# Performance work log

Measured on AMD Instinct MI355X. Metric: run time of the kernel, lower is better.

Reference implementation:

```python
import jax, jax.numpy as jnp
import numpy as np

B, L, E, D = 4, 1024, 128, 256
NPOI, EPOI, NH, FF = 10000, 128, 8, 256
HD = D // NH


def layer_norm(x, g, b, eps=1e-5):
    m = x.mean(-1, keepdims=True)
    v = ((x - m) ** 2).mean(-1, keepdims=True)
    return (x - m) / jnp.sqrt(v + eps) * g + b


def leaky_relu(x):
    return jnp.where(x >= 0, x, 0.01 * x)


def tokenize_timestamp(t):
    # t: (..., 2) = [timestamp_sec, delta_sec] -> (..., 4) = [week, hour, minute, d_minute]
    week = t[..., 0] % 604800.0 / 86400.0
    hour = t[..., 0] % 86400.0 / 3600.0
    minute = t[..., 0] % 3600.0 / 60.0
    return jnp.stack([week, hour, minute, t[..., 1] / 60.0], -1)


def pos_encode(pos, d):
    # standard sinusoidal PE evaluated at integer positions `pos`
    freq = jnp.exp(-jnp.log(10000.0) * (2.0 * jnp.arange(d // 2, dtype=jnp.float32)) / d)
    ang = pos[..., None].astype(jnp.float32) * freq  # (..., d/2)
    pe = jnp.zeros(pos.shape + (d,), jnp.float32)
    return pe.at[..., 0::2].set(jnp.sin(ang)).at[..., 1::2].set(jnp.cos(ang))


def setup_inputs():
    ks = iter(jax.random.split(jax.random.key(0), 48))

    def nrm(shape, s=0.02):
        return jax.random.normal(next(ks), shape, jnp.float32) * s

    spatial = jax.random.normal(next(ks), (B, L, 2), jnp.float32) * 10.0
    ts = jax.random.uniform(next(ks), (B, L), jnp.float32, 0.0, 1e6)
    dt = jax.random.uniform(next(ks), (B, L), jnp.float32, 0.0, 3600.0)
    token = jax.random.randint(next(ks), (B, L, 2), 0, 2).astype(jnp.float32)
    iq = jnp.zeros((B, L, 4, 2), jnp.float32)
    iq = iq.at[..., 0, 0].set(spatial[..., 0]).at[..., 1, 0].set(spatial[..., 1])
    iq = iq.at[..., 2, 0].set(ts).at[..., 3, 0].set(dt)
    iq = iq.at[..., 0, 1].set(token[..., 0]).at[..., 2, 1].set(token[..., 1])
    positions = jax.random.randint(next(ks), (B, L, 2), 0, L)
    return dict(
        input_seq=iq, positions=positions,
        poi_coors=jax.random.normal(next(ks), (NPOI, 2), jnp.float32) * 10.0,
        poi_embed_mat=nrm((NPOI, EPOI), 1.0),
        sp_w1=nrm((2, E)), sp_b1=jnp.zeros((E,), jnp.float32),
        sp_w2=nrm((E, D)), sp_b2=jnp.zeros((D,), jnp.float32),
        four_w=nrm((4, E), 1.0), four_b=nrm((4, E), 1.0),
        te_w=nrm((4 * E, D)), te_b=jnp.zeros((D,), jnp.float32),
        poi_ln_g=jnp.ones((EPOI,), jnp.float32), poi_ln_b=jnp.zeros((EPOI,), jnp.float32),
        poi_w=nrm((EPOI, D)), poi_b=jnp.zeros((D,), jnp.float32),
        tok_emb=nrm((6, E), 1.0).at[5].set(0.0),
        tok_ln_g=jnp.ones((E,), jnp.float32), tok_ln_b=jnp.zeros((E,), jnp.float32),
        tok_w=nrm((E, D)), tok_b=jnp.zeros((D,), jnp.float32),
        mha_in_w=nrm((D, 3 * D)), mha_in_b=jnp.zeros((3 * D,), jnp.float32),
        mha_out_w=nrm((D, D)), mha_out_b=jnp.zeros((D,), jnp.float32),
        ln1_g=jnp.ones((D,), jnp.float32), ln1_b=jnp.zeros((D,), jnp.float32),
        ff_w1=nrm((D, FF)), ff_b1=jnp.zeros((FF,), jnp.float32),
        ff_w2=nrm((FF, D)), ff_b2=jnp.zeros((D,), jnp.float32),
        ln2_g=jnp.ones((D,), jnp.float32), ln2_b=jnp.zeros((D,), jnp.float32))


def reference(input_seq, positions, poi_coors, poi_embed_mat,
              sp_w1, sp_b1, sp_w2, sp_b2, four_w, four_b, te_w, te_b,
              poi_ln_g, poi_ln_b, poi_w, poi_b,
              tok_emb, tok_ln_g, tok_ln_b, tok_w, tok_b,
              mha_in_w, mha_in_b, mha_out_w, mha_out_b,
              ln1_g, ln1_b, ff_w1, ff_b1, ff_w2, ff_b2, ln2_g, ln2_b):
    token = input_seq[..., jnp.array([0, 2]), 1].astype(jnp.int32)  # (B,L,2)
    spatial = input_seq[:, :, 0:2, 0]                                # (B,L,2)
    tt = tokenize_timestamp(input_seq[:, :, 2:4, 0])                 # (B,L,4)
    # token embedding: Embedding(6) -> LN -> Linear -> (B,L,2,D)
    tok_e = layer_norm(tok_emb[token], tok_ln_g, tok_ln_b) @ tok_w + tok_b
    # spatial embedding (note: original's masked_fill is non-inplace and discarded)
    sp_e = leaky_relu(spatial @ sp_w1 + sp_b1) @ sp_w2 + sp_b2 + tok_e[:, :, 0]
    # brute-force nearest POI: cdist^2 + argmin + gather
    d2 = ((poi_coors[None, None] - spatial[:, :, None]) ** 2).sum(-1)  # (B,L,NPOI)
    poi = jnp.argmin(d2, -1)                                           # (B,L)
    poi_e = layer_norm(poi_embed_mat[poi], poi_ln_g, poi_ln_b) @ poi_w + poi_b + tok_e[:, :, 0]
    # temporal: 4 FourierEncode modules -> concat -> LeakyReLU -> Linear
    t_e = jnp.cos(tt[..., None] * four_w + four_b).reshape(B, L, 4 * E)
    t_e = leaky_relu(t_e) @ te_w + te_b + tok_e[:, :, 1]
    # modal mixer: 1-layer post-norm TransformerEncoder over the 3 modalities
    x = jnp.stack([sp_e, t_e, poi_e], 2).reshape(B * L, 3, D)
    qkv = x @ mha_in_w + mha_in_b
    q, k, v = jnp.split(qkv, 3, -1)
    q = q.reshape(B * L, 3, NH, HD)
    k = k.reshape(B * L, 3, NH, HD)
    v = v.reshape(B * L, 3, NH, HD)
    att = jax.nn.softmax(jnp.einsum('nqhd,nkhd->nhqk', q, k) / jnp.sqrt(jnp.float32(HD)), -1)
    o = jnp.einsum('nhqk,nkhd->nqhd', att, v).reshape(B * L, 3, D) @ mha_out_w + mha_out_b
    x = layer_norm(x + o, ln1_g, ln1_b)
    x = layer_norm(x + (jax.nn.relu(x @ ff_w1 + ff_b1) @ ff_w2 + ff_b2), ln2_g, ln2_b)
    modal_h = x.reshape(B, L, 3, D).mean(2)
    modal_h = modal_h + pos_encode(positions[..., 0], D) + pos_encode(positions[..., 1], D)
    return modal_h  # == mem_seq in the original forward
```

## Files before the change

### kernel.cpp

```cpp
#include <hip/hip_runtime.h>
#include <math.h>

namespace {
constexpr int E = 128, D = 256;
constexpr int NPOI = 10000, NH = 8, FFD = 256;
constexpr int HD = D / NH;
constexpr int NTOK = 4096;
constexpr int TA = 4;
constexpr float LN_EPS = 1e-5f;

constexpr int PK_QKV = 0;
constexpr int PK_OUT = 196608;
constexpr int PK_FF1 = 262144;
constexpr int PK_FF2 = 327680;
constexpr int PK_E0  = 393216;
constexpr int PK_E1  = 458752;
constexpr int PK_E2  = 622592;
constexpr int PK_TOTAL = 688128;
constexpr int NTILES = PK_TOTAL / 512;
}

using frag8 = __attribute__((ext_vector_type(8))) short;
using f32x4 = __attribute__((ext_vector_type(4))) float;

__device__ __forceinline__ float bf2f(short s) {
    union { unsigned u; float f; } x; x.u = ((unsigned)(unsigned short)s) << 16; return x.f;
}
__device__ __forceinline__ unsigned short f2bf(float f) {
    union { float f; unsigned u; } x; x.f = f;
    unsigned r = x.u + 0x7fffu + ((x.u >> 16) & 1u);
    return (unsigned short)(r >> 16);
}

__device__ __forceinline__ float wsum64(float v) {
#pragma unroll
    for (int m = 1; m < 64; m <<= 1) v += __shfl_xor(v, m);
    return v;
}

__device__ __forceinline__ void ln128_bf(const float* __restrict__ src,
                                         const float* __restrict__ g,
                                         const float* __restrict__ b,
                                         short* __restrict__ dst1,
                                         short* __restrict__ dst2, int lane) {
    float v0 = src[lane], v1 = src[64 + lane];
    float mean = wsum64(v0 + v1) * (1.0f / 128.0f);
    float d0 = v0 - mean, d1 = v1 - mean;
    float var = wsum64(d0 * d0 + d1 * d1) * (1.0f / 128.0f);
    float inv = sqrtf(var + LN_EPS);
    float y0 = d0 / inv * g[lane] + b[lane];
    float y1 = d1 / inv * g[64 + lane] + b[64 + lane];
    unsigned short s0 = f2bf(y0), s1 = f2bf(y1);
    dst1[lane] = (short)s0; dst1[64 + lane] = (short)s1;
    if (dst2) { dst2[lane] = (short)s0; dst2[64 + lane] = (short)s1; }
}

__global__ __launch_bounds__(256)
void pack_weights(const float* __restrict__ wqkv, const float* __restrict__ wout,
                  const float* __restrict__ fw1,  const float* __restrict__ fw2,
                  const float* __restrict__ sp_w2, const float* __restrict__ te_w,
                  const float* __restrict__ poi_w, const float* __restrict__ tok_w,
                  unsigned short* __restrict__ pk)
{
    __shared__ float buf[4][32 * 17];
    const int wv = threadIdx.x >> 6, lane = threadIdx.x & 63;
    const int tile = blockIdx.x * 4 + wv;
    if (tile >= NTILES) return;

    int t = tile, sel, base;
    if (t < 384)              { sel = 0; base = PK_QKV; }
    else if ((t -= 384) < 128){ sel = 1; base = PK_OUT; }
    else if ((t -= 128) < 128){ sel = 2; base = PK_FF1; }
    else if ((t -= 128) < 128){ sel = 3; base = PK_FF2; }
    else if ((t -= 128) < 128){ sel = 4; base = PK_E0; }
    else if ((t -= 128) < 320){ sel = 5; base = PK_E1; }
    else                      { t -= 320; sel = 6; base = PK_E2; }
    const int NKT = (sel == 5) ? 20 : 8;
    const int nt = t / NKT, kt = t % NKT;

    const int k = kt * 32 + (lane >> 1);
    const int n0 = nt * 16 + (lane & 1) * 8;
    const float* row;
    switch (sel) {
        case 0:  row = wqkv + (size_t)k * 768; break;
        case 1:  row = wout + (size_t)k * 256; break;
        case 2:  row = fw1  + (size_t)k * 256; break;
        case 3:  row = fw2  + (size_t)k * 256; break;
        case 4:  row = (k < 128) ? sp_w2 + (size_t)k * 256 : tok_w + (size_t)(k - 128) * 256; break;
        case 5:  row = (k < 512) ? te_w  + (size_t)k * 256 : tok_w + (size_t)(k - 512) * 256; break;
        default: row = (k < 128) ? poi_w + (size_t)k * 256 : tok_w + (size_t)(k - 128) * 256; break;
    }
    float4 v0 = *(const float4*)(row + n0);
    float4 v1 = *(const float4*)(row + n0 + 4);
    float* b = buf[wv];
    const int wb = (lane >> 1) * 17 + (lane & 1) * 8;
    b[wb + 0] = v0.x; b[wb + 1] = v0.y; b[wb + 2] = v0.z; b[wb + 3] = v0.w;
    b[wb + 4] = v1.x; b[wb + 5] = v1.y; b[wb + 6] = v1.z; b[wb + 7] = v1.w;
    __syncthreads();

    const int rb = (lane >> 4) * 8, c = lane & 15;
    frag8 fr;
#pragma unroll
    for (int j = 0; j < 8; ++j) fr[j] = (short)f2bf(b[(rb + j) * 17 + c]);
    *(frag8*)(pk + base + ((size_t)t * 64 + lane) * 8) = fr;
}

__global__ __launch_bounds__(256, 4)
void embed_mfma(const float* __restrict__ iq,
                const float* __restrict__ poi_coors,
                const float* __restrict__ poi_embed,
                const float* __restrict__ sp_w1, const float* __restrict__ sp_b1,
                const float* __restrict__ sp_b2,
                const float* __restrict__ four_w, const float* __restrict__ four_b,
                const float* __restrict__ te_b,
                const float* __restrict__ poi_ln_g, const float* __restrict__ poi_ln_b,
                const float* __restrict__ poi_b,
                const float* __restrict__ tok_emb,
                const float* __restrict__ tok_ln_g, const float* __restrict__ tok_ln_b,
                const float* __restrict__ tok_b,
                const unsigned short* __restrict__ pk,
                unsigned short* __restrict__ xout)
{
    constexpr int P0 = 264, P1 = 648, P2 = 264;
    const int tid = threadIdx.x;
    const int w = tid >> 6, lane = tid & 63;
    const int quad = lane >> 4, l16 = lane & 15;
    const int n0 = blockIdx.x * TA;

    __shared__ __align__(16) char  U[25088];
    __shared__ float s_meta[TA][6];
    __shared__ int   s_tok[TA][2];
    __shared__ float s_wd[4][TA];
    __shared__ int   s_wi[4][TA];
    __shared__ int   s_poi[TA];

    short* h0 = (short*)U;
    short* h1 = (short*)U + 1056;
    short* h2 = (short*)U + 3648;

    if (tid < TA) {
        const float* p = iq + (size_t)(n0 + tid) * 8;
        s_meta[tid][0] = p[0];
        s_meta[tid][1] = p[2];
        float ts = p[4];
        float dt = p[6];
        s_tok[tid][0] = (int)p[1];
        s_tok[tid][1] = (int)p[5];
        s_meta[tid][2] = fmodf(ts, 604800.0f) / 86400.0f;
        s_meta[tid][3] = fmodf(ts, 86400.0f) / 3600.0f;
        s_meta[tid][4] = fmodf(ts, 3600.0f) / 60.0f;
        s_meta[tid][5] = dt / 60.0f;
    }
    __syncthreads();

    {
        float sx[TA], sy[TA], bd[TA];
        int bi[TA];
#pragma unroll
        for (int t = 0; t < TA; ++t) {
            sx[t] = s_meta[t][0]; sy[t] = s_meta[t][1];
            bd[t] = INFINITY; bi[t] = NPOI;
        }
        const float2* pc = (const float2*)poi_coors;
        for (int i = tid; i < NPOI; i += 256) {
            float2 p = pc[i];
#pragma unroll
            for (int t = 0; t < TA; ++t) {
                float dx = __fsub_rn(p.x, sx[t]);
                float dy = __fsub_rn(p.y, sy[t]);
                float d  = __fadd_rn(__fmul_rn(dx, dx), __fmul_rn(dy, dy));
                if (d < bd[t]) { bd[t] = d; bi[t] = i; }
            }
        }
#pragma unroll
        for (int m = 1; m < 64; m <<= 1) {
#pragma unroll
            for (int t = 0; t < TA; ++t) {
                float od = __shfl_xor(bd[t], m);
                int   oi = __shfl_xor(bi[t], m);
                if (od < bd[t] || (od == bd[t] && oi < bi[t])) { bd[t] = od; bi[t] = oi; }
            }
        }
        if (lane == 0) {
#pragma unroll
            for (int t = 0; t < TA; ++t) { s_wd[w][t] = bd[t]; s_wi[w][t] = bi[t]; }
        }
        __syncthreads();
        if (tid < TA) {
            float bdd = s_wd[0][tid]; int bii = s_wi[0][tid];
#pragma unroll
            for (int ww = 1; ww < 4; ++ww) {
                float od = s_wd[ww][tid]; int oi = s_wi[ww][tid];
                if (od < bdd || (od == bdd && oi < bii)) { bdd = od; bii = oi; }
            }
            s_poi[tid] = bii;
        }
        __syncthreads();
    }

    {
        const int t = w;
        ln128_bf(tok_emb + (size_t)s_tok[t][0] * E, tok_ln_g, tok_ln_b,
                 h0 + t * P0 + 128, h2 + t * P2 + 128, lane);
        ln128_bf(tok_emb + (size_t)s_tok[t][1] * E, tok_ln_g, tok_ln_b,
                 h1 + t * P1 + 512, nullptr, lane);
        ln128_bf(poi_embed + (size_t)s_poi[t] * E, poi_ln_g, poi_ln_b,
                 h2 + t * P2, nullptr, lane);
    }

    for (int idx = tid; idx < TA * 128; idx += 256) {
        int t = idx >> 7, l = idx & 127;
        float h = s_meta[t][0] * sp_w1[l] + s_meta[t][1] * sp_w1[128 + l] + sp_b1[l];
        h0[t * P0 + l] = (short)f2bf((h >= 0.0f) ? h : 0.01f * h);
    }
    for (int idx = tid; idx < TA * 512; idx += 256) {
        int t = idx >> 9, jj = idx & 511, f = jj >> 7;
        float c = cosf(s_meta[t][2 + f] * four_w[jj] + four_b[jj]);
        h1[t * P1 + jj] = (short)f2bf((c >= 0.0f) ? c : 0.01f * c);
    }
    __syncthreads();

    {
        f32x4 acc[4];
#pragma unroll
        for (int nt = 0; nt < 4; ++nt) {
            int c = w * 64 + nt * 16 + l16;
            float bv = sp_b2[c] + tok_b[c];
            acc[nt][0] = bv; acc[nt][1] = bv; acc[nt][2] = bv; acc[nt][3] = bv;
        }
        for (int kt = 0; kt < 8; ++kt) {
            frag8 a = *(const frag8*)(&h0[l16 * P0 + kt * 32 + quad * 8]);
#pragma unroll
            for (int nt = 0; nt < 4; ++nt) {
                frag8 b = *(const frag8*)(pk + PK_E0 + (((size_t)(w * 4 + nt) * 8 + kt) * 64 + lane) * 8);
                acc[nt] = __builtin_amdgcn_mfma_f32_16x16x32_bf16(a, b, acc[nt], 0, 0, 0);
            }
        }
        if (quad == 0) {
#pragma unroll
            for (int nt = 0; nt < 4; ++nt)
#pragma unroll
                for (int r = 0; r < 4; ++r)
                    xout[(size_t)(n0 + r) * 768 + w * 64 + nt * 16 + l16] = f2bf(acc[nt][r]);
        }
    }
    {
        f32x4 acc[4];
#pragma unroll
        for (int nt = 0; nt < 4; ++nt) {
            int c = w * 64 + nt * 16 + l16;
            float bv = te_b[c] + tok_b[c];
            acc[nt][0] = bv; acc[nt][1] = bv; acc[nt][2] = bv; acc[nt][3] = bv;
        }
        for (int kt = 0; kt < 20; ++kt) {
            frag8 a = *(const frag8*)(&h1[l16 * P1 + kt * 32 + quad * 8]);
#pragma unroll
            for (int nt = 0; nt < 4; ++nt) {
                frag8 b = *(const frag8*)(pk + PK_E1 + (((size_t)(w * 4 + nt) * 20 + kt) * 64 + lane) * 8);
                acc[nt] = __builtin_amdgcn_mfma_f32_16x16x32_bf16(a, b, acc[nt], 0, 0, 0);
            }
        }
        if (quad == 0) {
#pragma unroll
            for (int nt = 0; nt < 4; ++nt)
#pragma unroll
                for (int r = 0; r < 4; ++r)
                    xout[(size_t)(n0 + r) * 768 + 256 + w * 64 + nt * 16 + l16] = f2bf(acc[nt][r]);
        }
    }
    {
        f32x4 acc[4];
#pragma unroll
        for (int nt = 0; nt < 4; ++nt) {
            int c = w * 64 + nt * 16 + l16;
            float bv = poi_b[c] + tok_b[c];
            acc[nt][0] = bv; acc[nt][1] = bv; acc[nt][2] = bv; acc[nt][3] = bv;
        }
        for (int kt = 0; kt < 8; ++kt) {
            frag8 a = *(const frag8*)(&h2[l16 * P2 + kt * 32 + quad * 8]);
#pragma unroll
            for (int nt = 0; nt < 4; ++nt) {
                frag8 b = *(const frag8*)(pk + PK_E2 + (((size_t)(w * 4 + nt) * 8 + kt) * 64 + lane) * 8);
                acc[nt] = __builtin_amdgcn_mfma_f32_16x16x32_bf16(a, b, acc[nt], 0, 0, 0);
            }
        }
        if (quad == 0) {
#pragma unroll
            for (int nt = 0; nt < 4; ++nt)
#pragma unroll
                for (int r = 0; r < 4; ++r)
                    xout[(size_t)(n0 + r) * 768 + 512 + w * 64 + nt * 16 + l16] = f2bf(acc[nt][r]);
        }
    }
}

__global__ __launch_bounds__(256, 3)
void mha_ff_mfma(const unsigned short* __restrict__ xin,
                 const unsigned short* __restrict__ pk,
                 const float* __restrict__ bqkv, const float* __restrict__ bout,
                 const float* __restrict__ ln1g, const float* __restrict__ ln1b,
                 const float* __restrict__ fb1,  const float* __restrict__ fb2,
                 const float* __restrict__ ln2g, const float* __restrict__ ln2b,
                 const int* __restrict__ positions,
                 float* __restrict__ out)
{
    constexpr int PA = 264;
    constexpr int PQ = 776;
    constexpr int PF = 260;
    const int tid = threadIdx.x;
    const int w = tid >> 6, lane = tid & 63;
    const int quad = lane >> 4, l16 = lane & 15;
    const int n0tok = blockIdx.x * TA;
    const unsigned short* xg = xin + (size_t)n0tok * 3 * D;

    __shared__ __align__(16) short s_a[16 * PA];
    __shared__ __align__(16) char  U[25088];
    __shared__ float s_att[TA * NH * 9];

    short* qkv = (short*)U;
    float* s_f = (float*)U;
    short* s_h = (short*)(U + 16640);

    for (int i = tid; i < 12 * 32; i += 256) {
        int row = i >> 5, col = (i & 31) * 8;
        *(frag8*)(&s_a[row * PA + col]) = *(const frag8*)(xg + row * 256 + col);
    }
    __syncthreads();

    float xres[16];

    {
        f32x4 acc[12];
#pragma unroll
        for (int nt = 0; nt < 12; ++nt) {
            float bv = bqkv[w * 192 + nt * 16 + l16];
            acc[nt][0] = bv; acc[nt][1] = bv; acc[nt][2] = bv; acc[nt][3] = bv;
        }
        for (int kt = 0; kt < 8; ++kt) {
            frag8 a = *(const frag8*)(&s_a[l16 * PA + kt * 32 + quad * 8]);
#pragma unroll
            for (int nt = 0; nt < 12; ++nt) {
                frag8 b = *(const frag8*)(pk + PK_QKV + (((size_t)(w * 12 + nt) * 8 + kt) * 64 + lane) * 8);
                acc[nt] = __builtin_amdgcn_mfma_f32_16x16x32_bf16(a, b, acc[nt], 0, 0, 0);
            }
        }
#pragma unroll
        for (int nt = 0; nt < 4; ++nt)
#pragma unroll
            for (int r = 0; r < 4; ++r)
                xres[nt * 4 + r] = bf2f(s_a[(quad * 4 + r) * PA + w * 64 + nt * 16 + l16]);
#pragma unroll
        for (int nt = 0; nt < 12; ++nt)
#pragma unroll
            for (int r = 0; r < 4; ++r) {
                int row = quad * 4 + r, col = w * 192 + nt * 16 + l16;
                qkv[row * PQ + col] = (short)f2bf(acc[nt][r]);
            }
    }
    __syncthreads();

    for (int idx = tid; idx < TA * NH * 9; idx += 256) {
        int tok = idx / 72, rem = idx % 72;
        int h = rem / 9, qr = (rem % 9) / 3, kr = rem % 3;
        const short* qp = qkv + (tok * 3 + qr) * PQ + h * HD;
        const short* kp = qkv + (tok * 3 + kr) * PQ + D + h * HD;
        float s = 0.0f;
#pragma unroll
        for (int u = 0; u < HD; ++u) s += bf2f(qp[u]) * bf2f(kp[u]);
        s_att[idx] = s / sqrtf((float)HD);
    }
    __syncthreads();
    for (int idx3 = tid; idx3 < TA * NH * 3; idx3 += 256) {
        float* a = s_att + idx3 * 3;
        float m = fmaxf(a[0], fmaxf(a[1], a[2]));
        float e0 = expf(a[0] - m), e1 = expf(a[1] - m), e2 = expf(a[2] - m);
        float inv = 1.0f / (e0 + e1 + e2);
        a[0] = e0 * inv; a[1] = e1 * inv; a[2] = e2 * inv;
    }
    __syncthreads();

    {
        const int h = tid >> 5;
#pragma unroll
        for (int tok = 0; tok < TA; ++tok) {
            float v0 = bf2f(qkv[(tok * 3 + 0) * PQ + 2 * D + tid]);
            float v1 = bf2f(qkv[(tok * 3 + 1) * PQ + 2 * D + tid]);
            float v2 = bf2f(qkv[(tok * 3 + 2) * PQ + 2 * D + tid]);
#pragma unroll
            for (int qr = 0; qr < 3; ++qr) {
                const float* a = s_att + tok * 72 + h * 9 + qr * 3;
                s_a[(tok * 3 + qr) * PA + tid] = (short)f2bf(a[0] * v0 + a[1] * v1 + a[2] * v2);
            }
        }
    }
    __syncthreads();

    {
        f32x4 acc[4];
#pragma unroll
        for (int nt = 0; nt < 4; ++nt) {
            float bv = bout[w * 64 + nt * 16 + l16];
            acc[nt][0] = bv; acc[nt][1] = bv; acc[nt][2] = bv; acc[nt][3] = bv;
        }
        for (int kt = 0; kt < 8; ++kt) {
            frag8 a = *(const frag8*)(&s_a[l16 * PA + kt * 32 + quad * 8]);
#pragma unroll
            for (int nt = 0; nt < 4; ++nt) {
                frag8 b = *(const frag8*)(pk + PK_OUT + (((size_t)(w * 4 + nt) * 8 + kt) * 64 + lane) * 8);
                acc[nt] = __builtin_amdgcn_mfma_f32_16x16x32_bf16(a, b, acc[nt], 0, 0, 0);
            }
        }
        __syncthreads();
#pragma unroll
        for (int nt = 0; nt < 4; ++nt)
#pragma unroll
            for (int r = 0; r < 4; ++r) {
                int row = quad * 4 + r, col = w * 64 + nt * 16 + l16;
                s_f[row * PF + col] = acc[nt][r] + xres[nt * 4 + r];
            }
    }
    __syncthreads();

#pragma unroll
    for (int rr = 0; rr < 4; ++rr) {
        int row = w + rr * 4, col = lane * 4;
        float4 v = *(const float4*)(&s_f[row * PF + col]);
        float mean = wsum64(v.x + v.y + v.z + v.w) * (1.0f / 256.0f);
        float dx = v.x - mean, dy = v.y - mean, dz = v.z - mean, dw = v.w - mean;
        float var = wsum64(dx * dx + dy * dy + dz * dz + dw * dw) * (1.0f / 256.0f);
        float s = sqrtf(var + LN_EPS);
        float4 g = *(const float4*)(ln1g + col), b = *(const float4*)(ln1b + col);
        float y0 = dx / s * g.x + b.x, y1 = dy / s * g.y + b.y;
        float y2 = dz / s * g.z + b.z, y3 = dw / s * g.w + b.w;
        float4 yv; yv.x = y0; yv.y = y1; yv.z = y2; yv.w = y3;
        *(float4*)(&s_f[row * PF + col]) = yv;
        ushort4 bb; bb.x = f2bf(y0); bb.y = f2bf(y1); bb.z = f2bf(y2); bb.w = f2bf(y3);
        *(ushort4*)(&s_a[row * PA + col]) = bb;
    }
    __syncthreads();

    {
        f32x4 acc[4];
#pragma unroll
        for (int nt = 0; nt < 4; ++nt) {
            float bv = fb1[w * 64 + nt * 16 + l16];
            acc[nt][0] = bv; acc[nt][1] = bv; acc[nt][2] = bv; acc[nt][3] = bv;
        }
        for (int kt = 0; kt < 8; ++kt) {
            frag8 a = *(const frag8*)(&s_a[l16 * PA + kt * 32 + quad * 8]);
#pragma unroll
            for (int nt = 0; nt < 4; ++nt) {
                frag8 b = *(const frag8*)(pk + PK_FF1 + (((size_t)(w * 4 + nt) * 8 + kt) * 64 + lane) * 8);
                acc[nt] = __builtin_amdgcn_mfma_f32_16x16x32_bf16(a, b, acc[nt], 0, 0, 0);
            }
        }
#pragma unroll
        for (int nt = 0; nt < 4; ++nt)
#pragma unroll
            for (int r = 0; r < 4; ++r) {
                int row = quad * 4 + r, col = w * 64 + nt * 16 + l16;
                s_h[row * PA + col] = (short)f2bf(fmaxf(acc[nt][r], 0.0f));
            }
    }
    __syncthreads();

    {
        f32x4 acc[4];
#pragma unroll
        for (int nt = 0; nt < 4; ++nt) {
            float bv = fb2[w * 64 + nt * 16 + l16];
            acc[nt][0] = bv; acc[nt][1] = bv; acc[nt][2] = bv; acc[nt][3] = bv;
        }
        for (int kt = 0; kt < 8; ++kt) {
            frag8 a = *(const frag8*)(&s_h[l16 * PA + kt * 32 + quad * 8]);
#pragma unroll
            for (int nt = 0; nt < 4; ++nt) {
                frag8 b = *(const frag8*)(pk + PK_FF2 + (((size_t)(w * 4 + nt) * 8 + kt) * 64 + lane) * 8);
                acc[nt] = __builtin_amdgcn_mfma_f32_16x16x32_bf16(a, b, acc[nt], 0, 0, 0);
            }
        }
#pragma unroll
        for (int nt = 0; nt < 4; ++nt)
#pragma unroll
            for (int r = 0; r < 4; ++r) {
                int row = quad * 4 + r, col = w * 64 + nt * 16 + l16;
                float y = s_f[row * PF + col];
                s_f[row * PF + col] = acc[nt][r] + y;
            }
    }
    __syncthreads();

#pragma unroll
    for (int rr = 0; rr < 4; ++rr) {
        int row = w + rr * 4, col = lane * 4;
        float4 v = *(const float4*)(&s_f[row * PF + col]);
        float mean = wsum64(v.x + v.y + v.z + v.w) * (1.0f / 256.0f);
        float dx = v.x - mean, dy = v.y - mean, dz = v.z - mean, dw = v.w - mean;
        float var = wsum64(dx * dx + dy * dy + dz * dz + dw * dw) * (1.0f / 256.0f);
        float s = sqrtf(var + LN_EPS);
        float4 g = *(const float4*)(ln2g + col), b = *(const float4*)(ln2b + col);
        float4 zv;
        zv.x = dx / s * g.x + b.x; zv.y = dy / s * g.y + b.y;
        zv.z = dz / s * g.z + b.z; zv.w = dw / s * g.w + b.w;
        *(float4*)(&s_f[row * PF + col]) = zv;
    }
    __syncthreads();

    {
        const int fi = tid >> 1;
        const float freq = expf(-logf(10000.0f) * (2.0f * fi) / (float)D);
#pragma unroll
        for (int t = 0; t < TA; ++t) {
            int n = n0tok + t;
            float m3 = (s_f[(3 * t) * PF + tid] + s_f[(3 * t + 1) * PF + tid] +
                        s_f[(3 * t + 2) * PF + tid]) / 3.0f;
            float p0 = (float)positions[2 * n], p1 = (float)positions[2 * n + 1];
            float a0 = p0 * freq, a1 = p1 * freq;
            float pe = (tid & 1) ? (cosf(a0) + cosf(a1)) : (sinf(a0) + sinf(a1));
            out[(size_t)n * D + tid] = m3 + pe;
        }
    }
}

extern "C" void kernel_launch(void* const* d_in, const int* in_sizes, int n_in,
                              void* d_out, int out_size, void* d_ws, size_t ws_size,
                              hipStream_t stream)
{
    const float* iq        = (const float*)d_in[0];
    const int*   positions = (const int*)d_in[1];
    const float* poi_coors = (const float*)d_in[2];
    const float* poi_embed = (const float*)d_in[3];
    const float* sp_w1     = (const float*)d_in[4];
    const float* sp_b1     = (const float*)d_in[5];
    const float* sp_w2     = (const float*)d_in[6];
    const float* sp_b2     = (const float*)d_in[7];
    const float* four_w    = (const float*)d_in[8];
    const float* four_b    = (const float*)d_in[9];
    const float* te_w      = (const float*)d_in[10];
    const float* te_b      = (const float*)d_in[11];
    const float* poi_ln_g  = (const float*)d_in[12];
    const float* poi_ln_b  = (const float*)d_in[13];
    const float* poi_w     = (const float*)d_in[14];
    const float* poi_b     = (const float*)d_in[15];
    const float* tok_emb   = (const float*)d_in[16];
    const float* tok_ln_g  = (const float*)d_in[17];
    const float* tok_ln_b  = (const float*)d_in[18];
    const float* tok_w     = (const float*)d_in[19];
    const float* tok_b     = (const float*)d_in[20];
    const float* mha_in_w  = (const float*)d_in[21];
    const float* mha_in_b  = (const float*)d_in[22];
    const float* mha_out_w = (const float*)d_in[23];
    const float* mha_out_b = (const float*)d_in[24];
    const float* ln1_g     = (const float*)d_in[25];
    const float* ln1_b     = (const float*)d_in[26];
    const float* ff_w1     = (const float*)d_in[27];
    const float* ff_b1     = (const float*)d_in[28];
    const float* ff_w2     = (const float*)d_in[29];
    const float* ff_b2     = (const float*)d_in[30];
    const float* ln2_g     = (const float*)d_in[31];
    const float* ln2_b     = (const float*)d_in[32];

    unsigned short* pkw = (unsigned short*)d_ws;
    unsigned short* xws = (unsigned short*)((char*)d_ws + PK_TOTAL * 2);

    pack_weights<<<NTILES / 4, 256, 0, stream>>>(
        mha_in_w, mha_out_w, ff_w1, ff_w2, sp_w2, te_w, poi_w, tok_w, pkw);

    embed_mfma<<<NTOK / TA, 256, 0, stream>>>(
        iq, poi_coors, poi_embed, sp_w1, sp_b1, sp_b2, four_w, four_b, te_b,
        poi_ln_g, poi_ln_b, poi_b, tok_emb, tok_ln_g, tok_ln_b, tok_b,
        pkw, xws);

    mha_ff_mfma<<<NTOK / TA, 256, 0, stream>>>(
        xws, pkw, mha_in_b, mha_out_b, ln1_g, ln1_b,
        ff_b1, ff_b2, ln2_g, ln2_b, positions, (float*)d_out);
}
```

Measured before the change: 213.2 us.

## Stage embed output in LDS, fuse score+softmax, raise mha occupancy bound

The embedding kernel now writes its bf16 outputs into a shared-memory tile and then stores them to global memory with coalesced 16-byte vector writes, replacing scattered 2-byte stores. The attention score loop now has each thread compute all three key scores for a query and apply the softmax immediately, which removes one barrier and a shared-memory round trip. The MHA/FF kernel's launch bounds go from 3 to 4 waves per SIMD, which may push the compiler to spill registers. The extra LDS buffer adds about 6 KB per block in the embed kernel.

```diff
diff --git a/kernel.cpp b/kernel.cpp
--- a/kernel.cpp
+++ b/kernel.cpp
@@ -128,6 +128,7 @@
     const int n0 = blockIdx.x * TA;
 
     __shared__ __align__(16) char  U[25088];
+    __shared__ __align__(16) short s_x[TA * 768];
     __shared__ float s_meta[TA][6];
     __shared__ int   s_tok[TA][2];
     __shared__ float s_wd[4][TA];
@@ -241,7 +242,7 @@
             for (int nt = 0; nt < 4; ++nt)
 #pragma unroll
                 for (int r = 0; r < 4; ++r)
-                    xout[(size_t)(n0 + r) * 768 + w * 64 + nt * 16 + l16] = f2bf(acc[nt][r]);
+                    s_x[r * 768 + w * 64 + nt * 16 + l16] = (short)f2bf(acc[nt][r]);
         }
     }
     {
@@ -265,7 +266,7 @@
             for (int nt = 0; nt < 4; ++nt)
 #pragma unroll
                 for (int r = 0; r < 4; ++r)
-                    xout[(size_t)(n0 + r) * 768 + 256 + w * 64 + nt * 16 + l16] = f2bf(acc[nt][r]);
+                    s_x[r * 768 + 256 + w * 64 + nt * 16 + l16] = (short)f2bf(acc[nt][r]);
         }
     }
     {
@@ -289,12 +290,19 @@
             for (int nt = 0; nt < 4; ++nt)
 #pragma unroll
                 for (int r = 0; r < 4; ++r)
-                    xout[(size_t)(n0 + r) * 768 + 512 + w * 64 + nt * 16 + l16] = f2bf(acc[nt][r]);
-        }
-    }
-}
-
-__global__ __launch_bounds__(256, 3)
+                    s_x[r * 768 + 512 + w * 64 + nt * 16 + l16] = (short)f2bf(acc[nt][r]);
+        }
+    }
+    __syncthreads();
+
+    {
+        unsigned short* xg = xout + (size_t)n0 * 768;
+        for (int c = tid; c < TA * 96; c += 256)
+            *(frag8*)(xg + c * 8) = *(const frag8*)(&s_x[c * 8]);
+    }
+}
+
+__global__ __launch_bounds__(256, 4)
 void mha_ff_mfma(const unsigned short* __restrict__ xin,
                  const unsigned short* __restrict__ pk,
                  const float* __restrict__ bqkv, const float* __restrict__ bout,
@@ -359,23 +367,29 @@
     }
     __syncthreads();
 
-    for (int idx = tid; idx < TA * NH * 9; idx += 256) {
-        int tok = idx / 72, rem = idx % 72;
-        int h = rem / 9, qr = (rem % 9) / 3, kr = rem % 3;
+    for (int idx3 = tid; idx3 < TA * NH * 3; idx3 += 256) {
+        int tok = idx3 / 24, rem = idx3 % 24;
+        int h = rem / 3, qr = rem % 3;
         const short* qp = qkv + (tok * 3 + qr) * PQ + h * HD;
-        const short* kp = qkv + (tok * 3 + kr) * PQ + D + h * HD;
-        float s = 0.0f;
-#pragma unroll
-        for (int u = 0; u < HD; ++u) s += bf2f(qp[u]) * bf2f(kp[u]);
-        s_att[idx] = s / sqrtf((float)HD);
-    }
-    __syncthreads();
-    for (int idx3 = tid; idx3 < TA * NH * 3; idx3 += 256) {
-        float* a = s_att + idx3 * 3;
-        float m = fmaxf(a[0], fmaxf(a[1], a[2]));
-        float e0 = expf(a[0] - m), e1 = expf(a[1] - m), e2 = expf(a[2] - m);
+        const short* k0 = qkv + (tok * 3 + 0) * PQ + D + h * HD;
+        const short* k1 = qkv + (tok * 3 + 1) * PQ + D + h * HD;
+        const short* k2 = qkv + (tok * 3 + 2) * PQ + D + h * HD;
+        float s0 = 0.0f, s1 = 0.0f, s2 = 0.0f;
+#pragma unroll
+        for (int u = 0; u < HD; ++u) {
+            float q = bf2f(qp[u]);
+            s0 += q * bf2f(k0[u]);
+            s1 += q * bf2f(k1[u]);
+            s2 += q * bf2f(k2[u]);
+        }
+        const float sc = 1.0f / sqrtf((float)HD);
+        s0 *= sc; s1 *= sc; s2 *= sc;
+        float m = fmaxf(s0, fmaxf(s1, s2));
+        float e0 = expf(s0 - m), e1 = expf(s1 - m), e2 = expf(s2 - m);
         float inv = 1.0f / (e0 + e1 + e2);
-        a[0] = e0 * inv; a[1] = e1 * inv; a[2] = e2 * inv;
+        s_att[idx3 * 3 + 0] = e0 * inv;
+        s_att[idx3 * 3 + 1] = e1 * inv;
+        s_att[idx3 * 3 + 2] = e2 * inv;
     }
     __syncthreads();
 
```

New measurement: 211.7 us. No clear change (-0.7%).
